# Kernel optimization log

Measured on AMD Instinct MI355X. Metric: run time of the kernel, lower is better.

Reference implementation:

```python
import jax, jax.numpy as jnp
import numpy as np

T, B, D, H = 2048, 4, 1024, 16
HD = D // H  # head_dim = 64


def setup_inputs() -> dict:
    key = jax.random.key(0)
    ks = jax.random.split(key, 12)
    s = 1.0 / np.sqrt(D)
    return {
        "query": jax.random.normal(ks[0], (T, B, D), jnp.float32),
        "key": jax.random.normal(ks[1], (T, B, D), jnp.float32),
        "value": jax.random.normal(ks[2], (T, B, D), jnp.float32),
        "time_decay": jax.random.uniform(ks[3], (T, B, D), jnp.float32),
        "Wq": jax.random.normal(ks[4], (D, D), jnp.float32) * s,
        "bq": jax.random.normal(ks[5], (D,), jnp.float32) * s,
        "Wk": jax.random.normal(ks[6], (D, D), jnp.float32) * s,
        "bk": jax.random.normal(ks[7], (D,), jnp.float32) * s,
        "Wv": jax.random.normal(ks[8], (D, D), jnp.float32) * s,
        "bv": jax.random.normal(ks[9], (D,), jnp.float32) * s,
        "Wo": jax.random.normal(ks[10], (D, D), jnp.float32) * s,
        "bo": jax.random.normal(ks[11], (D,), jnp.float32) * s,
    }


def reference(query, key, value, time_decay, Wq, bq, Wk, bk, Wv, bv, Wo, bo):
    # Linear projections (torch Linear: x @ W.T + b). Inputs are (T, B, D).
    def split_heads(x, W, b):
        y = x @ W.T + b  # (T, B, D)
        # -> (B, H, T, HD)
        return y.reshape(T, B, H, HD).transpose(1, 2, 0, 3)

    Q = split_heads(query, Wq, bq)
    K = split_heads(key, Wk, bk)
    V = split_heads(value, Wv, bv)

    scale = 1.0 / np.sqrt(HD)
    scores = jnp.einsum("bhqd,bhkd->bhqk", Q, K) * scale  # (B, H, T, T)
    attn = jax.nn.softmax(scores, axis=-1)
    ctx = jnp.einsum("bhqk,bhkd->bhqd", attn, V)  # (B, H, T, HD)
    # -> (T, B, D)
    ctx = ctx.transpose(2, 0, 1, 3).reshape(T, B, D)
    out = ctx @ Wo.T + bo
    return out * time_decay
```

## Files before the change

### kernel.cpp

```cpp
#include <hip/hip_runtime.h>

#define TT 2048
#define BB 4
#define DD 1024
#define HH 16
#define HDIM 64
#define MM (TT*BB)

typedef __attribute__((ext_vector_type(4))) float float4v;
typedef _Float16 half8 __attribute__((ext_vector_type(8)));
typedef _Float16 half4 __attribute__((ext_vector_type(4)));
typedef _Float16 half2v __attribute__((ext_vector_type(2)));

static __device__ __forceinline__ half4 pk4(float a, float b, float c, float d) {
    half2v h0 = __builtin_bit_cast(half2v, __builtin_amdgcn_cvt_pkrtz(a, b));
    half2v h1 = __builtin_bit_cast(half2v, __builtin_amdgcn_cvt_pkrtz(c, d));
    half4 hv; hv[0]=h0[0]; hv[1]=h0[1]; hv[2]=h1[0]; hv[3]=h1[1];
    return hv;
}

static __device__ __forceinline__ float fexp2(float x) {
    float r; asm("v_exp_f32 %0, %1" : "=v"(r) : "v"(x)); return r;
}

#define GLD16(g, l) __builtin_amdgcn_global_load_lds( \
    (const __attribute__((address_space(1))) unsigned int*)(g), \
    (__attribute__((address_space(3))) unsigned int*)(l), 16, 0, 0)

__global__ __launch_bounds__(256) void cvt_f16(
    const float* __restrict__ q, const float* __restrict__ k, const float* __restrict__ v,
    const float* __restrict__ wq, const float* __restrict__ wk, const float* __restrict__ wv,
    const float* __restrict__ wo,
    _Float16* __restrict__ qh, _Float16* __restrict__ kh, _Float16* __restrict__ vh,
    _Float16* __restrict__ wqh, _Float16* __restrict__ wkh, _Float16* __restrict__ wvh,
    _Float16* __restrict__ woh)
{
    const int z = blockIdx.z;
    const float* src; _Float16* dst; int n;
    switch (z) {
        case 0: src=q;  dst=qh;  n=MM*DD/8; break;
        case 1: src=k;  dst=kh;  n=MM*DD/8; break;
        case 2: src=v;  dst=vh;  n=MM*DD/8; break;
        case 3: src=wq; dst=wqh; n=DD*DD/8; break;
        case 4: src=wk; dst=wkh; n=DD*DD/8; break;
        case 5: src=wv; dst=wvh; n=DD*DD/8; break;
        default: src=wo; dst=woh; n=DD*DD/8; break;
    }
    for (int c = blockIdx.x*blockDim.x + threadIdx.x; c < n; c += gridDim.x*blockDim.x) {
        const float4v* s4 = (const float4v*)src + (size_t)c*2;
        float4v a = s4[0], b = s4[1];
        *(half4*)(dst + (size_t)c*8)     = pk4(a[0],a[1],a[2],a[3]);
        *(half4*)(dst + (size_t)c*8 + 4) = pk4(b[0],b[1],b[2],b[3]);
    }
}

__global__ __launch_bounds__(256) void qkv_gemm(
    const _Float16* __restrict__ xq, const _Float16* __restrict__ xk, const _Float16* __restrict__ xv,
    const _Float16* __restrict__ wall,
    const float* __restrict__ bq, const float* __restrict__ bk, const float* __restrict__ bv,
    _Float16* __restrict__ dq, _Float16* __restrict__ dk, _Float16* __restrict__ dv)
{
    __shared__ __attribute__((aligned(16))) _Float16 As[2][128*64];
    __shared__ __attribute__((aligned(16))) _Float16 Bs[2][128*64];

    const int id   = blockIdx.x;
    const int wgid = (id & 7)*192 + (id >> 3);
    const int z    = wgid / 512;
    const int rem  = wgid & 511;
    const int by   = rem >> 3, bx = rem & 7;
    const int m0   = by*128, n0l = bx*128;

    const _Float16* X = (z==0)?xq:((z==1)?xk:xv);
    const float* Bb   = (z==0)?bq:((z==1)?bk:bv);
    _Float16* Dst     = (z==0)?dq:((z==1)?dk:dv);
    const float osc   = (z==0) ? 0.18033688011112042f : 1.0f;

    const int tid=threadIdx.x, lane=tid&63, w=tid>>6;
    const int wm=w>>1, wn=w&1;
    const int lrow=lane&15, lg=lane>>4;
    const int swzr = (lrow & 7) << 3;

    const int scol = ((lane&7) ^ (lane>>3))*8;
    const _Float16* ga = X    + (size_t)(m0 + w*32 + (lane>>3))*DD + scol;
    const _Float16* gb = wall + (size_t)(z*1024 + n0l + w*32 + (lane>>3))*DD + scol;

    float4v acc[4][4];
    for (int i=0;i<4;i++) for (int j=0;j<4;j++) acc[i][j]=(float4v){0.f,0.f,0.f,0.f};

    #pragma unroll
    for (int s=0;s<4;s++) GLD16(ga + (size_t)s*8*DD, &As[0][(w*32+s*8)*64]);
    #pragma unroll
    for (int s=0;s<4;s++) GLD16(gb + (size_t)s*8*DD, &Bs[0][(w*32+s*8)*64]);
    __syncthreads();

    for (int t=0; t<16; t++) {
        const int cb = t & 1, nb = cb ^ 1;
        if (t < 15) {
            const size_t k1 = (size_t)(t+1)*64;
            #pragma unroll
            for (int s=0;s<4;s++) GLD16(ga + (size_t)s*8*DD + k1, &As[nb][(w*32+s*8)*64]);
            #pragma unroll
            for (int s=0;s<4;s++) GLD16(gb + (size_t)s*8*DD + k1, &Bs[nb][(w*32+s*8)*64]);
        }
        #pragma unroll
        for (int kc=0;kc<2;kc++) {
            half8 a[4], b[4];
            #pragma unroll
            for (int i=0;i<4;i++) a[i] = *(const half8*)&As[cb][(wm*64+i*16+lrow)*64 + ((kc*32+lg*8) ^ swzr)];
            #pragma unroll
            for (int j=0;j<4;j++) b[j] = *(const half8*)&Bs[cb][(wn*64+j*16+lrow)*64 + ((kc*32+lg*8) ^ swzr)];
            #pragma unroll
            for (int i=0;i<4;i++)
            #pragma unroll
            for (int j=0;j<4;j++)
                acc[i][j] = __builtin_amdgcn_mfma_f32_16x16x32_f16(a[i], b[j], acc[i][j],0,0,0);
        }
        __syncthreads();
    }

    #pragma unroll
    for (int j=0;j<4;j++) {
        int n = n0l + wn*64 + j*16 + lrow;
        float bias = Bb[n];
        int h = n >> 6, hd = n & 63;
        #pragma unroll
        for (int i=0;i<4;i++)
        #pragma unroll
        for (int r=0;r<4;r++) {
            int m = m0 + wm*64 + i*16 + lg*4 + r;
            int tt = m >> 2, b = m & 3;
            Dst[((size_t)(b*HH + h)*TT + tt)*HDIM + hd] = (_Float16)((acc[i][j][r] + bias)*osc);
        }
    }
}

__global__ __launch_bounds__(256) void v_transpose(
    const _Float16* __restrict__ Vb, _Float16* __restrict__ VbT)
{
    const int tile = blockIdx.x;
    const int bh   = blockIdx.y;
    const int tid = threadIdx.x, tg = tid & 15, hg = tid >> 4;
    const int t0 = tile*64;

    half4 rv[4];
    #pragma unroll
    for (int r=0;r<4;r++)
        rv[r] = *(const half4*)(Vb + ((size_t)bh*TT + t0 + tg*4 + r)*HDIM + hg*4);
    #pragma unroll
    for (int c=0;c<4;c++) {
        half4 tv; tv[0]=rv[0][c]; tv[1]=rv[1][c]; tv[2]=rv[2][c]; tv[3]=rv[3][c];
        *(half4*)(VbT + ((size_t)bh*HDIM + hg*4 + c)*TT + t0 + tg*4) = tv;
    }
}

__global__ __launch_bounds__(256, 4) void attn(
    const _Float16* __restrict__ Qg, const _Float16* __restrict__ Kg,
    const _Float16* __restrict__ VT, _Float16* __restrict__ Ctx)
{
    __shared__ __attribute__((aligned(16))) _Float16 Kt[2][64*64];
    __shared__ __attribute__((aligned(16))) _Float16 Vs[2][64*64];

    const int id = blockIdx.x;
    const int bh = id & 63, qt = id >> 6;
    const int b = bh >> 4, h = bh & 15;
    const int tid = threadIdx.x, lane = tid & 63, w = tid >> 6;
    const int lrow = lane & 15, lg = lane >> 4;

    const _Float16* Qb  = Qg + ((size_t)bh*TT + qt*128)*HDIM;
    const _Float16* Kb  = Kg + (size_t)bh*TT*HDIM;
    const _Float16* Vtb = VT + (size_t)bh*HDIM*TT;

    const int srow = w*16 + (lane>>3);
    const int scol = ((lane&7) ^ (lane>>3))*8;

    half8 qf[2][2];
    #pragma unroll
    for (int i=0;i<2;i++)
    #pragma unroll
    for (int kc=0;kc<2;kc++)
        qf[i][kc] = *(const half8*)(Qb + (size_t)(w*32 + i*16 + lrow)*HDIM + kc*32 + lg*8);

    float4v oacc[2][4];
    for (int i=0;i<2;i++) for (int j=0;j<4;j++) oacc[i][j]=(float4v){0.f,0.f,0.f,0.f};
    float lsum[2] = {0.f, 0.f};

    #pragma unroll
    for (int s=0;s<2;s++) {
        GLD16(Kb  + (size_t)(srow + s*8)*HDIM + scol,        &Kt[0][(w*16 + s*8)*64]);
        GLD16(Vtb + (size_t)(srow + s*8)*TT   + scol,        &Vs[0][(w*16 + s*8)*64]);
    }
    __syncthreads();

    const int swz = (lrow & 7) << 3;

    for (int kt = 0; kt < 32; kt++) {
        const int cb = kt & 1, nb = cb ^ 1;

        if (kt < 31) {
            #pragma unroll
            for (int s=0;s<2;s++) {
                GLD16(Kb  + (size_t)((kt+1)*64 + srow + s*8)*HDIM + scol, &Kt[nb][(w*16 + s*8)*64]);
                GLD16(Vtb + (size_t)(srow + s*8)*TT + (kt+1)*64 + scol,   &Vs[nb][(w*16 + s*8)*64]);
            }
        }

        float4v st[4][2];
        #pragma unroll
        for (int j=0;j<4;j++) for (int i=0;i<2;i++) st[j][i]=(float4v){0.f,0.f,0.f,0.f};
        #pragma unroll
        for (int kc=0;kc<2;kc++) {
            half8 kf[4];
            #pragma unroll
            for (int j=0;j<4;j++)
                kf[j] = *(const half8*)&Kt[cb][(j*16 + lrow)*64 + ((kc*32 + lg*8) ^ swz)];
            __builtin_amdgcn_s_setprio(1);
            #pragma unroll
            for (int j=0;j<4;j++)
            #pragma unroll
            for (int i=0;i<2;i++)
                st[j][i] = __builtin_amdgcn_mfma_f32_16x16x32_f16(kf[j], qf[i][kc], st[j][i],0,0,0);
            __builtin_amdgcn_s_setprio(0);
        }

        #pragma unroll
        for (int j=0;j<4;j++) {
            half4 pa[2];
            #pragma unroll
            for (int i=0;i<2;i++) {
                float p0 = fexp2(st[j][i][0]);
                float p1 = fexp2(st[j][i][1]);
                float p2 = fexp2(st[j][i][2]);
                float p3 = fexp2(st[j][i][3]);
                lsum[i] += (p0+p1)+(p2+p3);
                pa[i] = pk4(p0,p1,p2,p3);
            }
            half4 vf[4];
            #pragma unroll
            for (int jo=0;jo<4;jo++)
                vf[jo] = *(const half4*)&Vs[cb][(jo*16 + lrow)*64 + ((j*16 + lg*4) ^ swz)];
            __builtin_amdgcn_s_setprio(1);
            #pragma unroll
            for (int i=0;i<2;i++)
            #pragma unroll
            for (int jo=0;jo<4;jo++)
                oacc[i][jo] = __builtin_amdgcn_mfma_f32_16x16x16f16(vf[jo], pa[i], oacc[i][jo],0,0,0);
            __builtin_amdgcn_s_setprio(0);
        }

        __syncthreads();
    }

    #pragma unroll
    for (int i=0;i<2;i++) {
        float s = lsum[i];
        s += __shfl_xor(s, 16, 64);
        s += __shfl_xor(s, 32, 64);
        lsum[i] = s;
    }

    #pragma unroll
    for (int i=0;i<2;i++) {
        float inv = 1.f / lsum[i];
        int t = qt*128 + w*32 + i*16 + lrow;
        _Float16* crow = Ctx + ((size_t)t*BB + b)*DD + h*HDIM;
        #pragma unroll
        for (int jo=0;jo<4;jo++) {
            *(half4*)(crow + jo*16 + lg*4) =
                pk4(oacc[i][jo][0]*inv, oacc[i][jo][1]*inv,
                    oacc[i][jo][2]*inv, oacc[i][jo][3]*inv);
        }
    }
}

__global__ __launch_bounds__(256) void out_gemm(
    const _Float16* __restrict__ Cx, const _Float16* __restrict__ Woh,
    const float* __restrict__ bo, const float* __restrict__ td,
    float* __restrict__ Out)
{
    __shared__ __attribute__((aligned(16))) _Float16 As[2][128*64];
    __shared__ __attribute__((aligned(16))) _Float16 Bs[2][128*64];

    const int id   = blockIdx.x;
    const int wgid = (id & 7)*64 + (id >> 3);
    const int by   = wgid >> 3, bx = wgid & 7;
    const int m0   = by*128, n0 = bx*128;

    const int tid=threadIdx.x, lane=tid&63, w=tid>>6;
    const int wm=w>>1, wn=w&1;
    const int lrow=lane&15, lg=lane>>4;
    const int swzr = (lrow & 7) << 3;

    const int scol = ((lane&7) ^ (lane>>3))*8;
    const _Float16* ga = Cx  + (size_t)(m0 + w*32 + (lane>>3))*DD + scol;
    const _Float16* gb = Woh + (size_t)(n0 + w*32 + (lane>>3))*DD + scol;

    float4v acc[4][4];
    for (int i=0;i<4;i++) for (int j=0;j<4;j++) acc[i][j]=(float4v){0.f,0.f,0.f,0.f};

    #pragma unroll
    for (int s=0;s<4;s++) GLD16(ga + (size_t)s*8*DD, &As[0][(w*32+s*8)*64]);
    #pragma unroll
    for (int s=0;s<4;s++) GLD16(gb + (size_t)s*8*DD, &Bs[0][(w*32+s*8)*64]);
    __syncthreads();

    for (int t=0; t<16; t++) {
        const int cb = t & 1, nb = cb ^ 1;
        if (t < 15) {
            const size_t k1 = (size_t)(t+1)*64;
            #pragma unroll
            for (int s=0;s<4;s++) GLD16(ga + (size_t)s*8*DD + k1, &As[nb][(w*32+s*8)*64]);
            #pragma unroll
            for (int s=0;s<4;s++) GLD16(gb + (size_t)s*8*DD + k1, &Bs[nb][(w*32+s*8)*64]);
        }
        #pragma unroll
        for (int kc=0;kc<2;kc++) {
            half8 a[4], b[4];
            #pragma unroll
            for (int i=0;i<4;i++) a[i] = *(const half8*)&As[cb][(wm*64+i*16+lrow)*64 + ((kc*32+lg*8) ^ swzr)];
            #pragma unroll
            for (int j=0;j<4;j++) b[j] = *(const half8*)&Bs[cb][(wn*64+j*16+lrow)*64 + ((kc*32+lg*8) ^ swzr)];
            #pragma unroll
            for (int i=0;i<4;i++)
            #pragma unroll
            for (int j=0;j<4;j++)
                acc[i][j] = __builtin_amdgcn_mfma_f32_16x16x32_f16(a[i], b[j], acc[i][j],0,0,0);
        }
        __syncthreads();
    }

    #pragma unroll
    for (int j=0;j<4;j++) {
        int n = n0 + wn*64 + j*16 + lrow;
        float bias = bo[n];
        #pragma unroll
        for (int i=0;i<4;i++)
        #pragma unroll
        for (int r=0;r<4;r++) {
            int m = m0 + wm*64 + i*16 + lg*4 + r;
            size_t off = (size_t)m*DD + n;
            Out[off] = (acc[i][j][r] + bias) * td[off];
        }
    }
}

extern "C" void kernel_launch(void* const* d_in, const int* in_sizes, int n_in,
                              void* d_out, int out_size, void* d_ws, size_t ws_size,
                              hipStream_t stream) {
    const float* q  = (const float*)d_in[0];
    const float* k  = (const float*)d_in[1];
    const float* v  = (const float*)d_in[2];
    const float* td = (const float*)d_in[3];
    const float* Wq = (const float*)d_in[4];
    const float* bq = (const float*)d_in[5];
    const float* Wk = (const float*)d_in[6];
    const float* bk = (const float*)d_in[7];
    const float* Wv = (const float*)d_in[8];
    const float* bv = (const float*)d_in[9];
    const float* Wo = (const float*)d_in[10];
    const float* bo = (const float*)d_in[11];
    float* out = (float*)d_out;

    _Float16* qh  = (_Float16*)d_ws;
    _Float16* kh  = qh  + (size_t)MM*DD;
    _Float16* vh  = kh  + (size_t)MM*DD;
    _Float16* wqh = vh  + (size_t)MM*DD;
    _Float16* wkh = wqh + (size_t)DD*DD;
    _Float16* wvh = wkh + (size_t)DD*DD;
    _Float16* woh = wvh + (size_t)DD*DD;
    _Float16* Qb  = woh + (size_t)DD*DD;
    _Float16* Kb  = Qb  + (size_t)MM*DD;
    _Float16* Vb  = Kb  + (size_t)MM*DD;
    _Float16* VbT = vh;
    _Float16* Cx  = qh;

    cvt_f16    <<<dim3(2048,1,7), 256, 0, stream>>>(q,k,v, Wq,Wk,Wv,Wo, qh,kh,vh, wqh,wkh,wvh,woh);
    qkv_gemm   <<<dim3(1536),     256, 0, stream>>>(qh,kh,vh, wqh, bq,bk,bv, Qb,Kb,Vb);
    v_transpose<<<dim3(32,64),    256, 0, stream>>>(Vb, VbT);
    attn       <<<dim3(1024),     256, 0, stream>>>(Qb, Kb, VbT, Cx);
    out_gemm   <<<dim3(512),      256, 0, stream>>>(Cx, woh, bo, td, out);
}
```

Before: 371.5 us.

## Halve GEMM K-tile to 32 for higher occupancy and unroll double-buffer loops

The QKV and output GEMMs now use a K-step of 32 instead of 64. That halves shared memory per block (32KB instead of 64KB), with a new 4-lane XOR swizzle, and adds launch_bounds(256,4) to allow more resident workgroups. All three pipelined loops, including attention, are manually unrolled by two with separate named buffers so buffer indices are compile-time constants. The trade-off is twice as many barriers and global-load issue points per GEMM, and possible register pressure under the occupancy bound.

```diff
diff --git a/kernel.cpp b/kernel.cpp
--- a/kernel.cpp
+++ b/kernel.cpp
@@ -54,14 +54,14 @@
     }
 }
 
-__global__ __launch_bounds__(256) void qkv_gemm(
+__global__ __launch_bounds__(256, 4) void qkv_gemm(
     const _Float16* __restrict__ xq, const _Float16* __restrict__ xk, const _Float16* __restrict__ xv,
     const _Float16* __restrict__ wall,
     const float* __restrict__ bq, const float* __restrict__ bk, const float* __restrict__ bv,
     _Float16* __restrict__ dq, _Float16* __restrict__ dk, _Float16* __restrict__ dv)
 {
-    __shared__ __attribute__((aligned(16))) _Float16 As[2][128*64];
-    __shared__ __attribute__((aligned(16))) _Float16 Bs[2][128*64];
+    __shared__ __attribute__((aligned(16))) _Float16 As0[128*32], As1[128*32];
+    __shared__ __attribute__((aligned(16))) _Float16 Bs0[128*32], Bs1[128*32];
 
     const int id   = blockIdx.x;
     const int wgid = (id & 7)*192 + (id >> 3);
@@ -78,45 +78,48 @@
     const int tid=threadIdx.x, lane=tid&63, w=tid>>6;
     const int wm=w>>1, wn=w&1;
     const int lrow=lane&15, lg=lane>>4;
-    const int swzr = (lrow & 7) << 3;
-
-    const int scol = ((lane&7) ^ (lane>>3))*8;
-    const _Float16* ga = X    + (size_t)(m0 + w*32 + (lane>>3))*DD + scol;
-    const _Float16* gb = wall + (size_t)(z*1024 + n0l + w*32 + (lane>>3))*DD + scol;
+    const int swA = (lg ^ (lrow&3))*8;
+
+    const int gsl = ((lane&3) ^ ((lane>>2)&3))*8;
+    const _Float16* ga = X    + (size_t)(m0 + w*32 + (lane>>2))*DD + gsl;
+    const _Float16* gb = wall + (size_t)(z*1024 + n0l + w*32 + (lane>>2))*DD + gsl;
 
     float4v acc[4][4];
     for (int i=0;i<4;i++) for (int j=0;j<4;j++) acc[i][j]=(float4v){0.f,0.f,0.f,0.f};
 
-    #pragma unroll
-    for (int s=0;s<4;s++) GLD16(ga + (size_t)s*8*DD, &As[0][(w*32+s*8)*64]);
-    #pragma unroll
-    for (int s=0;s<4;s++) GLD16(gb + (size_t)s*8*DD, &Bs[0][(w*32+s*8)*64]);
+    GLD16(ga,                 As0 + (w*32)*32);
+    GLD16(ga + (size_t)16*DD, As0 + (w*32+16)*32);
+    GLD16(gb,                 Bs0 + (w*32)*32);
+    GLD16(gb + (size_t)16*DD, Bs0 + (w*32+16)*32);
     __syncthreads();
 
-    for (int t=0; t<16; t++) {
-        const int cb = t & 1, nb = cb ^ 1;
-        if (t < 15) {
-            const size_t k1 = (size_t)(t+1)*64;
-            #pragma unroll
-            for (int s=0;s<4;s++) GLD16(ga + (size_t)s*8*DD + k1, &As[nb][(w*32+s*8)*64]);
-            #pragma unroll
-            for (int s=0;s<4;s++) GLD16(gb + (size_t)s*8*DD + k1, &Bs[nb][(w*32+s*8)*64]);
-        }
-        #pragma unroll
-        for (int kc=0;kc<2;kc++) {
-            half8 a[4], b[4];
-            #pragma unroll
-            for (int i=0;i<4;i++) a[i] = *(const half8*)&As[cb][(wm*64+i*16+lrow)*64 + ((kc*32+lg*8) ^ swzr)];
-            #pragma unroll
-            for (int j=0;j<4;j++) b[j] = *(const half8*)&Bs[cb][(wn*64+j*16+lrow)*64 + ((kc*32+lg*8) ^ swzr)];
-            #pragma unroll
-            for (int i=0;i<4;i++)
-            #pragma unroll
-            for (int j=0;j<4;j++)
-                acc[i][j] = __builtin_amdgcn_mfma_f32_16x16x32_f16(a[i], b[j], acc[i][j],0,0,0);
-        }
-        __syncthreads();
-    }
+#define QSTEP(T, CA, CB_, NA, NB_, PREF)                                      \
+    {                                                                         \
+        if (PREF) {                                                           \
+            const size_t kk = (size_t)((T)+1)*32;                             \
+            GLD16(ga + kk,                 NA + (w*32)*32);                   \
+            GLD16(ga + (size_t)16*DD + kk, NA + (w*32+16)*32);                \
+            GLD16(gb + kk,                 NB_ + (w*32)*32);                  \
+            GLD16(gb + (size_t)16*DD + kk, NB_ + (w*32+16)*32);               \
+        }                                                                     \
+        half8 a[4], b[4];                                                     \
+        _Pragma("unroll")                                                     \
+        for (int i=0;i<4;i++) a[i] = *(const half8*)&CA[(wm*64+i*16+lrow)*32 + swA];  \
+        _Pragma("unroll")                                                     \
+        for (int j=0;j<4;j++) b[j] = *(const half8*)&CB_[(wn*64+j*16+lrow)*32 + swA]; \
+        _Pragma("unroll")                                                     \
+        for (int i=0;i<4;i++)                                                 \
+        _Pragma("unroll")                                                     \
+        for (int j=0;j<4;j++)                                                 \
+            acc[i][j] = __builtin_amdgcn_mfma_f32_16x16x32_f16(a[i], b[j], acc[i][j],0,0,0); \
+        __syncthreads();                                                      \
+    }
+
+    for (int t=0; t<32; t+=2) {
+        QSTEP(t,   As0, Bs0, As1, Bs1, 1);
+        QSTEP(t+1, As1, Bs1, As0, Bs0, (t+2)<32);
+    }
+#undef QSTEP
 
     #pragma unroll
     for (int j=0;j<4;j++) {
@@ -157,8 +160,8 @@
     const _Float16* __restrict__ Qg, const _Float16* __restrict__ Kg,
     const _Float16* __restrict__ VT, _Float16* __restrict__ Ctx)
 {
-    __shared__ __attribute__((aligned(16))) _Float16 Kt[2][64*64];
-    __shared__ __attribute__((aligned(16))) _Float16 Vs[2][64*64];
+    __shared__ __attribute__((aligned(16))) _Float16 Kt0[64*64], Kt1[64*64];
+    __shared__ __attribute__((aligned(16))) _Float16 Vs0[64*64], Vs1[64*64];
 
     const int id = blockIdx.x;
     const int bh = id & 63, qt = id >> 6;
@@ -186,69 +189,71 @@
 
     #pragma unroll
     for (int s=0;s<2;s++) {
-        GLD16(Kb  + (size_t)(srow + s*8)*HDIM + scol,        &Kt[0][(w*16 + s*8)*64]);
-        GLD16(Vtb + (size_t)(srow + s*8)*TT   + scol,        &Vs[0][(w*16 + s*8)*64]);
+        GLD16(Kb  + (size_t)(srow + s*8)*HDIM + scol, Kt0 + (w*16 + s*8)*64);
+        GLD16(Vtb + (size_t)(srow + s*8)*TT   + scol, Vs0 + (w*16 + s*8)*64);
     }
     __syncthreads();
 
     const int swz = (lrow & 7) << 3;
 
-    for (int kt = 0; kt < 32; kt++) {
-        const int cb = kt & 1, nb = cb ^ 1;
-
-        if (kt < 31) {
-            #pragma unroll
-            for (int s=0;s<2;s++) {
-                GLD16(Kb  + (size_t)((kt+1)*64 + srow + s*8)*HDIM + scol, &Kt[nb][(w*16 + s*8)*64]);
-                GLD16(Vtb + (size_t)(srow + s*8)*TT + (kt+1)*64 + scol,   &Vs[nb][(w*16 + s*8)*64]);
-            }
-        }
-
-        float4v st[4][2];
-        #pragma unroll
-        for (int j=0;j<4;j++) for (int i=0;i<2;i++) st[j][i]=(float4v){0.f,0.f,0.f,0.f};
-        #pragma unroll
-        for (int kc=0;kc<2;kc++) {
-            half8 kf[4];
-            #pragma unroll
-            for (int j=0;j<4;j++)
-                kf[j] = *(const half8*)&Kt[cb][(j*16 + lrow)*64 + ((kc*32 + lg*8) ^ swz)];
-            __builtin_amdgcn_s_setprio(1);
-            #pragma unroll
-            for (int j=0;j<4;j++)
-            #pragma unroll
-            for (int i=0;i<2;i++)
-                st[j][i] = __builtin_amdgcn_mfma_f32_16x16x32_f16(kf[j], qf[i][kc], st[j][i],0,0,0);
-            __builtin_amdgcn_s_setprio(0);
-        }
-
-        #pragma unroll
-        for (int j=0;j<4;j++) {
-            half4 pa[2];
-            #pragma unroll
-            for (int i=0;i<2;i++) {
-                float p0 = fexp2(st[j][i][0]);
-                float p1 = fexp2(st[j][i][1]);
-                float p2 = fexp2(st[j][i][2]);
-                float p3 = fexp2(st[j][i][3]);
-                lsum[i] += (p0+p1)+(p2+p3);
-                pa[i] = pk4(p0,p1,p2,p3);
-            }
-            half4 vf[4];
-            #pragma unroll
-            for (int jo=0;jo<4;jo++)
-                vf[jo] = *(const half4*)&Vs[cb][(jo*16 + lrow)*64 + ((j*16 + lg*4) ^ swz)];
-            __builtin_amdgcn_s_setprio(1);
-            #pragma unroll
-            for (int i=0;i<2;i++)
-            #pragma unroll
-            for (int jo=0;jo<4;jo++)
-                oacc[i][jo] = __builtin_amdgcn_mfma_f32_16x16x16f16(vf[jo], pa[i], oacc[i][jo],0,0,0);
-            __builtin_amdgcn_s_setprio(0);
-        }
-
-        __syncthreads();
-    }
+#define ASTEP(KT, CK, CV, NK, NV, PREF)                                       \
+    {                                                                         \
+        if (PREF) {                                                           \
+            _Pragma("unroll")                                                 \
+            for (int s=0;s<2;s++) {                                           \
+                GLD16(Kb  + (size_t)(((KT)+1)*64 + srow + s*8)*HDIM + scol, NK + (w*16 + s*8)*64); \
+                GLD16(Vtb + (size_t)(srow + s*8)*TT + ((KT)+1)*64 + scol,   NV + (w*16 + s*8)*64); \
+            }                                                                 \
+        }                                                                     \
+        float4v st[4][2];                                                     \
+        _Pragma("unroll")                                                     \
+        for (int j=0;j<4;j++) for (int i=0;i<2;i++) st[j][i]=(float4v){0.f,0.f,0.f,0.f}; \
+        _Pragma("unroll")                                                     \
+        for (int kc=0;kc<2;kc++) {                                            \
+            half8 kf[4];                                                      \
+            _Pragma("unroll")                                                 \
+            for (int j=0;j<4;j++)                                             \
+                kf[j] = *(const half8*)&CK[(j*16 + lrow)*64 + ((kc*32 + lg*8) ^ swz)]; \
+            __builtin_amdgcn_s_setprio(1);                                    \
+            _Pragma("unroll")                                                 \
+            for (int j=0;j<4;j++)                                             \
+            _Pragma("unroll")                                                 \
+            for (int i=0;i<2;i++)                                             \
+                st[j][i] = __builtin_amdgcn_mfma_f32_16x16x32_f16(kf[j], qf[i][kc], st[j][i],0,0,0); \
+            __builtin_amdgcn_s_setprio(0);                                    \
+        }                                                                     \
+        _Pragma("unroll")                                                     \
+        for (int j=0;j<4;j++) {                                               \
+            half4 pa[2];                                                      \
+            _Pragma("unroll")                                                 \
+            for (int i=0;i<2;i++) {                                           \
+                float p0 = fexp2(st[j][i][0]);                                \
+                float p1 = fexp2(st[j][i][1]);                                \
+                float p2 = fexp2(st[j][i][2]);                                \
+                float p3 = fexp2(st[j][i][3]);                                \
+                lsum[i] += (p0+p1)+(p2+p3);                                   \
+                pa[i] = pk4(p0,p1,p2,p3);                                     \
+            }                                                                 \
+            half4 vf[4];                                                      \
+            _Pragma("unroll")                                                 \
+            for (int jo=0;jo<4;jo++)                                          \
+                vf[jo] = *(const half4*)&CV[(jo*16 + lrow)*64 + ((j*16 + lg*4) ^ swz)]; \
+            __builtin_amdgcn_s_setprio(1);                                    \
+            _Pragma("unroll")                                                 \
+            for (int i=0;i<2;i++)                                             \
+            _Pragma("unroll")                                                 \
+            for (int jo=0;jo<4;jo++)                                          \
+                oacc[i][jo] = __builtin_amdgcn_mfma_f32_16x16x16f16(vf[jo], pa[i], oacc[i][jo],0,0,0); \
+            __builtin_amdgcn_s_setprio(0);                                    \
+        }                                                                     \
+        __syncthreads();                                                      \
+    }
+
+    for (int kt = 0; kt < 32; kt += 2) {
+        ASTEP(kt,   Kt0, Vs0, Kt1, Vs1, 1);
+        ASTEP(kt+1, Kt1, Vs1, Kt0, Vs0, (kt+2)<32);
+    }
+#undef ASTEP
 
     #pragma unroll
     for (int i=0;i<2;i++) {
@@ -272,13 +277,13 @@
     }
 }
 
-__global__ __launch_bounds__(256) void out_gemm(
+__global__ __launch_bounds__(256, 4) void out_gemm(
     const _Float16* __restrict__ Cx, const _Float16* __restrict__ Woh,
     const float* __restrict__ bo, const float* __restrict__ td,
     float* __restrict__ Out)
 {
-    __shared__ __attribute__((aligned(16))) _Float16 As[2][128*64];
-    __shared__ __attribute__((aligned(16))) _Float16 Bs[2][128*64];
+    __shared__ __attribute__((aligned(16))) _Float16 As0[128*32], As1[128*32];
+    __shared__ __attribute__((aligned(16))) _Float16 Bs0[128*32], Bs1[128*32];
 
     const int id   = blockIdx.x;
     const int wgid = (id & 7)*64 + (id >> 3);
@@ -288,45 +293,48 @@
     const int tid=threadIdx.x, lane=tid&63, w=tid>>6;
     const int wm=w>>1, wn=w&1;
     const int lrow=lane&15, lg=lane>>4;
-    const int swzr = (lrow & 7) << 3;
-
-    const int scol = ((lane&7) ^ (lane>>3))*8;
-    const _Float16* ga = Cx  + (size_t)(m0 + w*32 + (lane>>3))*DD + scol;
-    const _Float16* gb = Woh + (size_t)(n0 + w*32 + (lane>>3))*DD + scol;
+    const int swA = (lg ^ (lrow&3))*8;
+
+    const int gsl = ((lane&3) ^ ((lane>>2)&3))*8;
+    const _Float16* ga = Cx  + (size_t)(m0 + w*32 + (lane>>2))*DD + gsl;
+    const _Float16* gb = Woh + (size_t)(n0 + w*32 + (lane>>2))*DD + gsl;
 
     float4v acc[4][4];
     for (int i=0;i<4;i++) for (int j=0;j<4;j++) acc[i][j]=(float4v){0.f,0.f,0.f,0.f};
 
-    #pragma unroll
-    for (int s=0;s<4;s++) GLD16(ga + (size_t)s*8*DD, &As[0][(w*32+s*8)*64]);
-    #pragma unroll
-    for (int s=0;s<4;s++) GLD16(gb + (size_t)s*8*DD, &Bs[0][(w*32+s*8)*64]);
+    GLD16(ga,                 As0 + (w*32)*32);
+    GLD16(ga + (size_t)16*DD, As0 + (w*32+16)*32);
+    GLD16(gb,                 Bs0 + (w*32)*32);
+    GLD16(gb + (size_t)16*DD, Bs0 + (w*32+16)*32);
     __syncthreads();
 
-    for (int t=0; t<16; t++) {
-        const int cb = t & 1, nb = cb ^ 1;
-        if (t < 15) {
-            const size_t k1 = (size_t)(t+1)*64;
-            #pragma unroll
-            for (int s=0;s<4;s++) GLD16(ga + (size_t)s*8*DD + k1, &As[nb][(w*32+s*8)*64]);
-            #pragma unroll
-            for (int s=0;s<4;s++) GLD16(gb + (size_t)s*8*DD + k1, &Bs[nb][(w*32+s*8)*64]);
-        }
-        #pragma unroll
-        for (int kc=0;kc<2;kc++) {
-            half8 a[4], b[4];
-            #pragma unroll
-            for (int i=0;i<4;i++) a[i] = *(const half8*)&As[cb][(wm*64+i*16+lrow)*64 + ((kc*32+lg*8) ^ swzr)];
-            #pragma unroll
-            for (int j=0;j<4;j++) b[j] = *(const half8*)&Bs[cb][(wn*64+j*16+lrow)*64 + ((kc*32+lg*8) ^ swzr)];
-            #pragma unroll
-            for (int i=0;i<4;i++)
-            #pragma unroll
-            for (int j=0;j<4;j++)
-                acc[i][j] = __builtin_amdgcn_mfma_f32_16x16x32_f16(a[i], b[j], acc[i][j],0,0,0);
-        }
-        __syncthreads();
-    }
+#define OSTEP(T, CA, CB_, NA, NB_, PREF)                                      \
+    {                                                                         \
+        if (PREF) {                                                           \
+            const size_t kk = (size_t)((T)+1)*32;                             \
+            GLD16(ga + kk,                 NA + (w*32)*32);                   \
+            GLD16(ga + (size_t)16*DD + kk, NA + (w*32+16)*32);                \
+            GLD16(gb + kk,                 NB_ + (w*32)*32);                  \
+            GLD16(gb + (size_t)16*DD + kk, NB_ + (w*32+16)*32);               \
+        }                                                                     \
+        half8 a[4], b[4];                                                     \
+        _Pragma("unroll")                                                     \
+        for (int i=0;i<4;i++) a[i] = *(const half8*)&CA[(wm*64+i*16+lrow)*32 + swA];  \
+        _Pragma("unroll")                                                     \
+        for (int j=0;j<4;j++) b[j] = *(const half8*)&CB_[(wn*64+j*16+lrow)*32 + swA]; \
+        _Pragma("unroll")                                                     \
+        for (int i=0;i<4;i++)                                                 \
+        _Pragma("unroll")                                                     \
+        for (int j=0;j<4;j++)                                                 \
+            acc[i][j] = __builtin_amdgcn_mfma_f32_16x16x32_f16(a[i], b[j], acc[i][j],0,0,0); \
+        __syncthreads();                                                      \
+    }
+
+    for (int t=0; t<32; t+=2) {
+        OSTEP(t,   As0, Bs0, As1, Bs1, 1);
+        OSTEP(t+1, As1, Bs1, As0, Bs0, (t+2)<32);
+    }
+#undef OSTEP
 
     #pragma unroll
     for (int j=0;j<4;j++) {
```

After: 389.6 us. 1.05x slower.
